# Performance work log

Measured on AMD Instinct MI355X. Metric: run time of the kernel, lower is better.

The kernel has to match this reference:

```python
import jax, jax.numpy as jnp
import numpy as np

B, L, H, E = 8, 1024, 8, 64  # self-attention: S=L, D=E
SCALE = 1.0 / np.sqrt(E).astype(np.float32)


def setup_inputs() -> dict:
    key = jax.random.key(0)
    ks = jax.random.split(key, 6)
    shp = (B, L, H, E)
    names = ["q_re", "q_im", "k_re", "k_im", "v_re", "v_im"]
    return {n: jax.random.normal(k, shp, dtype=jnp.float32) for n, k in zip(names, ks)}


def reference(q_re, q_im, k_re, k_im, v_re, v_im):
    q = jax.lax.complex(q_re, q_im)  # [B,L,H,E] complex64
    k = jax.lax.complex(k_re, k_im)  # [B,S,H,E] complex64
    # complex QK^T (no conjugate, matching torch einsum semantics)
    scores = jnp.einsum('blhe,bshe->bhls', q, k)      # [B,H,L,S] complex64
    A = jax.nn.softmax(SCALE * jnp.abs(scores), axis=-1)  # [B,H,L,S] real
    # A is promoted to complex with zero imaginary part in the original;
    # multiplying complex V by a real A is equivalent per real/imag part.
    V_re = jnp.einsum('bhls,bshd->blhd', A, v_re)     # [B,L,H,D]
    V_im = jnp.einsum('bhls,bshd->blhd', A, v_im)     # [B,L,H,D]
    return jnp.stack([V_re, V_im], axis=-1)           # [B,L,H,D,2] (re, im)
```

## Files before the change

### kernel.cpp

```cpp
#include <hip/hip_runtime.h>


#define B_ 8
#define L_ 1024
#define H_ 8
#define E_ 64
#define SB 64
#define QB 128
#define NT 16
#define IMG_BYTES 32768
#define WS_NEEDED (64ull * NT * IMG_BYTES)
#define C_EXP 0.18033688011112042f

typedef float  f32x4  __attribute__((ext_vector_type(4)));
typedef float  f32x16 __attribute__((ext_vector_type(16)));
typedef __bf16 bf16x8 __attribute__((ext_vector_type(8)));
typedef unsigned short u16x8 __attribute__((ext_vector_type(8)));
typedef unsigned short u16x4 __attribute__((ext_vector_type(4)));
typedef unsigned int   u32x4 __attribute__((ext_vector_type(4)));

static __device__ __forceinline__ unsigned short f2b(float f) {
    __bf16 h = (__bf16)f;
    return __builtin_bit_cast(unsigned short, h);
}

static __device__ __forceinline__ float fsqrt_(float x) {
    return __builtin_amdgcn_sqrtf(x);
}
static __device__ __forceinline__ float fexp2_(float x) {
    return __builtin_amdgcn_exp2f(x);
}

static __device__ __forceinline__ u16x8 pack8(float4 a, float4 b) {
    u16x8 t;
    t[0]=f2b(a.x); t[1]=f2b(a.y); t[2]=f2b(a.z); t[3]=f2b(a.w);
    t[4]=f2b(b.x); t[5]=f2b(b.y); t[6]=f2b(b.z); t[7]=f2b(b.w);
    return t;
}

static __device__ __forceinline__ f32x16 mfma32(u16x8 a, u16x8 b, f32x16 c) {
    return __builtin_amdgcn_mfma_f32_32x32x16_bf16(
        __builtin_bit_cast(bf16x8, a), __builtin_bit_cast(bf16x8, b), c, 0, 0, 0);
}

static __device__ __forceinline__ unsigned int cvtpk(float lo, float hi) {
    unsigned int r;
    asm("v_cvt_pk_bf16_f32 %0, %1, %2" : "=v"(r) : "v"(lo), "v"(hi));
    return r;
}

static __device__ __forceinline__ void plswap(unsigned int& x, unsigned int& y) {
    asm("v_permlane32_swap_b32 %0, %1" : "+v"(x), "+v"(y));
}

static __device__ __forceinline__ u16x8 negbf8(u16x8 a) {
    u32x4 u = __builtin_bit_cast(u32x4, a);
    u[0] ^= 0x80008000u; u[1] ^= 0x80008000u; u[2] ^= 0x80008000u; u[3] ^= 0x80008000u;
    return __builtin_bit_cast(u16x8, u);
}

static __device__ __forceinline__ void qk_half(
    const u16x8 K[8], const u16x8 qre[4], const u16x8 qim[4],
    f32x16& sR, f32x16& sI)
{
    const f32x16 z16 = {};
    __builtin_amdgcn_s_setprio(1);
    sR = mfma32(K[0], qre[0], z16);
    sI = mfma32(K[1], qre[0], z16);
    sR = mfma32(K[1], negbf8(qim[0]), sR);
    sI = mfma32(K[0], qim[0], sI);
    sR = mfma32(K[2], qre[1], sR);
    sI = mfma32(K[3], qre[1], sI);
    sR = mfma32(K[3], negbf8(qim[1]), sR);
    sI = mfma32(K[2], qim[1], sI);
    sR = mfma32(K[4], qre[2], sR);
    sI = mfma32(K[5], qre[2], sI);
    sR = mfma32(K[5], negbf8(qim[2]), sR);
    sI = mfma32(K[4], qim[2], sI);
    sR = mfma32(K[6], qre[3], sR);
    sI = mfma32(K[7], qre[3], sI);
    sR = mfma32(K[7], negbf8(qim[3]), sR);
    sI = mfma32(K[6], qim[3], sI);
    __builtin_amdgcn_s_setprio(0);
}

static __device__ __forceinline__ void sm_half(
    f32x16 sR, f32x16 sI, float& lsum, u16x8& pa0, u16x8& pa1)
{
    float p[16];
#pragma unroll
    for (int r = 0; r < 16; ++r) {
        float mag = fsqrt_(fmaf(sR[r], sR[r], sI[r] * sI[r]));
        p[r] = fexp2_(mag * C_EXP);
    }
    lsum += (((p[0]+p[1])+(p[2]+p[3])) + ((p[4]+p[5])+(p[6]+p[7])))
          + (((p[8]+p[9])+(p[10]+p[11])) + ((p[12]+p[13])+(p[14]+p[15])));

    unsigned int a0 = cvtpk(p[0],  p[1]),  a1 = cvtpk(p[4],  p[5]);
    unsigned int a2 = cvtpk(p[2],  p[3]),  a3 = cvtpk(p[6],  p[7]);
    unsigned int b0 = cvtpk(p[8],  p[9]),  b1 = cvtpk(p[12], p[13]);
    unsigned int b2 = cvtpk(p[10], p[11]), b3 = cvtpk(p[14], p[15]);
    plswap(a0, a1);
    plswap(a2, a3);
    plswap(b0, b1);
    plswap(b2, b3);
    u32x4 wa = {a0, a2, a1, a3};
    u32x4 wb = {b0, b2, b1, b3};
    pa0 = __builtin_bit_cast(u16x8, wa);
    pa1 = __builtin_bit_cast(u16x8, wb);
}

static __device__ __forceinline__ void pv_half(
    u16x8 pa0, u16x8 pa1, const u16x8 vf[8],
    f32x16& oR0, f32x16& oR1, f32x16& oI0, f32x16& oI1)
{
    __builtin_amdgcn_s_setprio(1);
    oR0 = mfma32(pa0, vf[0], oR0);
    oR1 = mfma32(pa0, vf[1], oR1);
    oI0 = mfma32(pa0, vf[2], oI0);
    oI1 = mfma32(pa0, vf[3], oI1);
    oR0 = mfma32(pa1, vf[4], oR0);
    oR1 = mfma32(pa1, vf[5], oR1);
    oI0 = mfma32(pa1, vf[6], oI0);
    oI1 = mfma32(pa1, vf[7], oI1);
    __builtin_amdgcn_s_setprio(0);
}

__global__ __launch_bounds__(256) void ffa_prepack(
    const float* __restrict__ k_re, const float* __restrict__ k_im,
    const float* __restrict__ v_re, const float* __restrict__ v_im,
    char* __restrict__ ws)
{
    const int tid = threadIdx.x;
    const int bh  = blockIdx.x >> 4;
    const int st  = blockIdx.x & 15;
    const int b   = bh >> 3;
    const int h   = bh & 7;
    const int s0  = st * SB;
    char* const img = ws + (size_t)blockIdx.x * IMG_BYTES;

    const int l   = tid & 63;
    const int fg  = tid >> 6;
    const int l31 = l & 31;
    const int lh  = l >> 5;

#pragma unroll
    for (int ff = 0; ff < 8; ++ff) {
        const int f = fg * 8 + ff;
        u16x8 val;
        if (f < 16) {
            const int kh = f >> 3, ks = (f >> 1) & 3, c = f & 1;
            const float* src = (c ? k_im : k_re)
                + ((size_t)((b * L_ + s0 + kh * 32 + l31) * H_ + h)) * E_ + ks * 16 + lh * 8;
            const float4* p = (const float4*)src;
            val = pack8(p[0], p[1]);
        } else {
            const int g = f - 16, ks = g >> 2, j = g & 3;
            const float* src = (j >= 2) ? v_im : v_re;
            const int d = (j & 1) * 32 + l31;
            const int sb = s0 + ks * 16 + lh * 8;
            float4 t0, t1;
            t0.x = src[((size_t)((b * L_ + sb + 0) * H_ + h)) * E_ + d];
            t0.y = src[((size_t)((b * L_ + sb + 1) * H_ + h)) * E_ + d];
            t0.z = src[((size_t)((b * L_ + sb + 2) * H_ + h)) * E_ + d];
            t0.w = src[((size_t)((b * L_ + sb + 3) * H_ + h)) * E_ + d];
            t1.x = src[((size_t)((b * L_ + sb + 4) * H_ + h)) * E_ + d];
            t1.y = src[((size_t)((b * L_ + sb + 5) * H_ + h)) * E_ + d];
            t1.z = src[((size_t)((b * L_ + sb + 6) * H_ + h)) * E_ + d];
            t1.w = src[((size_t)((b * L_ + sb + 7) * H_ + h)) * E_ + d];
            val = pack8(t0, t1);
        }
        *(u16x8*)(img + f * 1024 + l * 16) = val;
    }
}

__global__ __launch_bounds__(256, 2) void ffa_main(
    const float* __restrict__ q_re, const float* __restrict__ q_im,
    const char* __restrict__ ws, float* __restrict__ out)
{
    const int tid  = threadIdx.x;
    const int lane = tid & 63;
    const int w    = tid >> 6;
    const int l31  = lane & 31;
    const int h    = lane >> 5;

    const int work = (blockIdx.x & 7) * 64 + (blockIdx.x >> 3);
    const int bh   = work >> 3;
    const int qblk = work & 7;
    const int b    = bh >> 3;
    const int hh   = bh & 7;
    const char* const imgs = ws + (size_t)bh * (NT * IMG_BYTES) + lane * 16;

    u16x8 kc[8], kn[8], vf[8];
#pragma unroll
    for (int j = 0; j < 8; ++j)
        kc[j] = *(const u16x8*)(imgs + j * 1024);
    __builtin_amdgcn_sched_barrier(0);

    u16x8 qre[4], qim[4];
    {
        const int qrow = qblk * QB + w * 32 + l31;
        const int base = ((b * L_ + qrow) * H_ + hh) * E_;
#pragma unroll
        for (int ks = 0; ks < 4; ++ks) {
            const float4* pr = (const float4*)(q_re + base + ks * 16 + h * 8);
            const float4* pi = (const float4*)(q_im + base + ks * 16 + h * 8);
            qre[ks] = pack8(pr[0], pr[1]);
            qim[ks] = pack8(pi[0], pi[1]);
        }
    }

    f32x16 oR0 = {}, oR1 = {}, oI0 = {}, oI1 = {};
    float lsum = 0.f;

    for (int t = 0; t < NT; ++t) {
        const char* const tb0 = imgs + (size_t)t * IMG_BYTES;
        const char* const tb1 = tb0 + IMG_BYTES;

#pragma unroll
        for (int g = 0; g < 8; ++g)
            vf[g] = *(const u16x8*)(tb0 + (16 + g) * 1024);
#pragma unroll
        for (int j = 0; j < 8; ++j)
            kn[j] = *(const u16x8*)(tb0 + 8192 + j * 1024);
        __builtin_amdgcn_sched_barrier(0);
        {
            f32x16 sR, sI;
            qk_half(kc, qre, qim, sR, sI);
            u16x8 pa0, pa1;
            sm_half(sR, sI, lsum, pa0, pa1);
            pv_half(pa0, pa1, vf, oR0, oR1, oI0, oI1);
        }

#pragma unroll
        for (int g = 0; g < 8; ++g)
            vf[g] = *(const u16x8*)(tb0 + (24 + g) * 1024);
        if (t < NT - 1) {
#pragma unroll
            for (int j = 0; j < 8; ++j)
                kc[j] = *(const u16x8*)(tb1 + j * 1024);
        }
        __builtin_amdgcn_sched_barrier(0);
        {
            f32x16 sR, sI;
            qk_half(kn, qre, qim, sR, sI);
            u16x8 pa0, pa1;
            sm_half(sR, sI, lsum, pa0, pa1);
            pv_half(pa0, pa1, vf, oR0, oR1, oI0, oI1);
        }
    }

    lsum += __shfl_xor(lsum, 32);
    const float inv = 1.0f / lsum;
#pragma unroll
    for (int r = 0; r < 16; ++r) {
        const int qs = (r & 3) + 8 * (r >> 2) + 4 * h;
        const float iv = __shfl(inv, qs);
        const int lq = qblk * QB + w * 32 + qs;
        float* op = out + ((b * L_ + lq) * H_ + hh) * (E_ * 2);
        float2 v0 = make_float2(oR0[r] * iv, oI0[r] * iv);
        float2 v1 = make_float2(oR1[r] * iv, oI1[r] * iv);
        *(float2*)(op + l31 * 2)      = v0;
        *(float2*)(op + 64 + l31 * 2) = v1;
    }
}

__global__ __launch_bounds__(256) void ffa_fwd_fb(
    const float* __restrict__ q_re, const float* __restrict__ q_im,
    const float* __restrict__ k_re, const float* __restrict__ k_im,
    const float* __restrict__ v_re, const float* __restrict__ v_im,
    float* __restrict__ out)
{
    __shared__ __align__(16) unsigned short Kt[64 * 128];
    __shared__ __align__(16) unsigned short Vt[128 * 64];
    __shared__ __align__(16) unsigned short Pw[4 * 16 * 64];
    char* const kb = (char*)Kt;
    char* const vb = (char*)Vt;

    const int tid  = threadIdx.x;
    const int lane = tid & 63;
    const int w    = tid >> 6;
    const int lr   = lane & 15;
    const int lg   = lane >> 4;
    const int lg16 = lg * 16;
    const int qblk = blockIdx.x & 15;
    const int bh   = blockIdx.x >> 4;
    const int b    = bh >> 3;
    const int h    = bh & 7;

    u16x8 qre[2], qim[2], qimn[2];
    {
        const int qrow = qblk * 64 + w * 16 + lr;
        const int base = ((b * L_ + qrow) * H_ + h) * E_ + lg * 8;
#pragma unroll
        for (int ks = 0; ks < 2; ++ks) {
            const float4* pr = (const float4*)(q_re + base + ks * 32);
            const float4* pi = (const float4*)(q_im + base + ks * 32);
            qre[ks] = pack8(pr[0], pr[1]);
            qim[ks] = pack8(pi[0], pi[1]);
#pragma unroll
            for (int i = 0; i < 8; ++i)
                qimn[ks][i] = (unsigned short)(qim[ks][i] ^ 0x8000u);
        }
    }

    float lsum[4];
    f32x4 Ore[4], Oim[4];
    const f32x4 zero = {0.f, 0.f, 0.f, 0.f};
#pragma unroll
    for (int r = 0; r < 4; ++r) lsum[r] = 0.f;
#pragma unroll
    for (int dt = 0; dt < 4; ++dt) { Ore[dt] = zero; Oim[dt] = zero; }

    const int sr = tid >> 2;
    const int sc = (tid & 3) * 16;
    const int vtens = tid >> 7;
    const int vd    = ((tid >> 4) & 7) * 8;
    const int vs    = (tid & 15) * 4;
    const float* const vsrc = vtens ? v_im : v_re;

    for (int st = 0; st < L_ / SB; ++st) {
        const int s0 = st * SB;
        {
            const int kg = ((b * L_ + s0 + sr) * H_ + h) * E_ + sc;
            const float4* pr = (const float4*)(k_re + kg);
            const float4* pi = (const float4*)(k_im + kg);
            float4 r0 = pr[0], r1 = pr[1], r2 = pr[2], r3 = pr[3];
            float4 i0 = pi[0], i1 = pi[1], i2 = pi[2], i3 = pi[3];
            const int krow = sr * 256;
            const int ksw  = (sr & 7) << 4;
            *(u16x8*)(kb + ((krow + sc * 2           ) ^ ksw)) = pack8(r0, r1);
            *(u16x8*)(kb + ((krow + sc * 2 + 16      ) ^ ksw)) = pack8(r2, r3);
            *(u16x8*)(kb + ((krow + 128 + sc * 2     ) ^ ksw)) = pack8(i0, i1);
            *(u16x8*)(kb + ((krow + 128 + sc * 2 + 16) ^ ksw)) = pack8(i2, i3);
        }
        {
            float vv[4][8];
#pragma unroll
            for (int j = 0; j < 4; ++j) {
                const float4* p = (const float4*)(vsrc + ((b * L_ + s0 + vs + j) * H_ + h) * E_ + vd);
                float4 x = p[0], y = p[1];
                vv[j][0]=x.x; vv[j][1]=x.y; vv[j][2]=x.z; vv[j][3]=x.w;
                vv[j][4]=y.x; vv[j][5]=y.y; vv[j][6]=y.z; vv[j][7]=y.w;
            }
#pragma unroll
            for (int i = 0; i < 8; ++i) {
                const int row = vtens * 64 + vd + i;
                u16x4 t;
                t[0]=f2b(vv[0][i]); t[1]=f2b(vv[1][i]); t[2]=f2b(vv[2][i]); t[3]=f2b(vv[3][i]);
                *(u16x4*)(vb + ((row * 128 + vs * 2) ^ ((row & 7) << 4))) = t;
            }
        }
        __syncthreads();

        f32x4 aR[4], aI[4];
#pragma unroll
        for (int t = 0; t < 4; ++t) { aR[t] = zero; aI[t] = zero; }
#pragma unroll
        for (int t = 0; t < 4; ++t) {
            const int key = t * 16 + lr;
            const char* kr = kb + key * 256;
            const int sw = (key & 7) << 4;
            u16x8 br0 = *(const u16x8*)(kr + (( lg16      ) ^ sw));
            u16x8 br1 = *(const u16x8*)(kr + (( 64 + lg16 ) ^ sw));
            u16x8 bi0 = *(const u16x8*)(kr + ((128 + lg16 ) ^ sw));
            u16x8 bi1 = *(const u16x8*)(kr + ((192 + lg16 ) ^ sw));
            aR[t] = __builtin_amdgcn_mfma_f32_16x16x32_bf16(__builtin_bit_cast(bf16x8,qre[0]),  __builtin_bit_cast(bf16x8,br0), aR[t],0,0,0);
            aR[t] = __builtin_amdgcn_mfma_f32_16x16x32_bf16(__builtin_bit_cast(bf16x8,qre[1]),  __builtin_bit_cast(bf16x8,br1), aR[t],0,0,0);
            aR[t] = __builtin_amdgcn_mfma_f32_16x16x32_bf16(__builtin_bit_cast(bf16x8,qimn[0]), __builtin_bit_cast(bf16x8,bi0), aR[t],0,0,0);
            aR[t] = __builtin_amdgcn_mfma_f32_16x16x32_bf16(__builtin_bit_cast(bf16x8,qimn[1]), __builtin_bit_cast(bf16x8,bi1), aR[t],0,0,0);
            aI[t] = __builtin_amdgcn_mfma_f32_16x16x32_bf16(__builtin_bit_cast(bf16x8,qre[0]),  __builtin_bit_cast(bf16x8,bi0), aI[t],0,0,0);
            aI[t] = __builtin_amdgcn_mfma_f32_16x16x32_bf16(__builtin_bit_cast(bf16x8,qre[1]),  __builtin_bit_cast(bf16x8,bi1), aI[t],0,0,0);
            aI[t] = __builtin_amdgcn_mfma_f32_16x16x32_bf16(__builtin_bit_cast(bf16x8,qim[0]),  __builtin_bit_cast(bf16x8,br0), aI[t],0,0,0);
            aI[t] = __builtin_amdgcn_mfma_f32_16x16x32_bf16(__builtin_bit_cast(bf16x8,qim[1]),  __builtin_bit_cast(bf16x8,br1), aI[t],0,0,0);
        }

        float p_[4][4];
#pragma unroll
        for (int t = 0; t < 4; ++t)
#pragma unroll
            for (int r = 0; r < 4; ++r) {
                float re = aR[t][r], im = aI[t][r];
                p_[t][r] = fexp2_(fsqrt_(fmaf(re, re, im * im)) * C_EXP);
            }
#pragma unroll
        for (int r = 0; r < 4; ++r)
            lsum[r] += (p_[0][r] + p_[1][r]) + (p_[2][r] + p_[3][r]);

        char* const pb = (char*)Pw + w * 2048;
#pragma unroll
        for (int t = 0; t < 4; ++t)
#pragma unroll
            for (int r = 0; r < 4; ++r) {
                const int prow = lg * 4 + r;
                *(unsigned short*)(pb + ((prow * 128 + (t * 16 + lr) * 2) ^ ((prow & 7) << 4)))
                    = f2b(p_[t][r]);
            }
        asm volatile("s_waitcnt lgkmcnt(0)" ::: "memory");
        __builtin_amdgcn_sched_barrier(0);
        const int psw = (lr & 7) << 4;
        u16x8 pf0 = *(const u16x8*)(pb + ((lr * 128 + lg16     ) ^ psw));
        u16x8 pf1 = *(const u16x8*)(pb + ((lr * 128 + 64 + lg16) ^ psw));

#pragma unroll
        for (int dt = 0; dt < 4; ++dt) {
            const int dr = dt * 16 + lr;
            const int swr = (dr & 7) << 4;
            const char* vrre = vb + dr * 128;
            const char* vrim = vb + (64 + dr) * 128;
            u16x8 vr0 = *(const u16x8*)(vrre + (( lg16     ) ^ swr));
            u16x8 vr1 = *(const u16x8*)(vrre + (( 64 + lg16) ^ swr));
            u16x8 vi0 = *(const u16x8*)(vrim + (( lg16     ) ^ swr));
            u16x8 vi1 = *(const u16x8*)(vrim + (( 64 + lg16) ^ swr));
            Ore[dt] = __builtin_amdgcn_mfma_f32_16x16x32_bf16(__builtin_bit_cast(bf16x8,pf0), __builtin_bit_cast(bf16x8,vr0), Ore[dt],0,0,0);
            Ore[dt] = __builtin_amdgcn_mfma_f32_16x16x32_bf16(__builtin_bit_cast(bf16x8,pf1), __builtin_bit_cast(bf16x8,vr1), Ore[dt],0,0,0);
            Oim[dt] = __builtin_amdgcn_mfma_f32_16x16x32_bf16(__builtin_bit_cast(bf16x8,pf0), __builtin_bit_cast(bf16x8,vi0), Oim[dt],0,0,0);
            Oim[dt] = __builtin_amdgcn_mfma_f32_16x16x32_bf16(__builtin_bit_cast(bf16x8,pf1), __builtin_bit_cast(bf16x8,vi1), Oim[dt],0,0,0);
        }
        __syncthreads();
    }

#pragma unroll
    for (int r = 0; r < 4; ++r) {
        float s = lsum[r];
        s += __shfl_xor(s, 1);
        s += __shfl_xor(s, 2);
        s += __shfl_xor(s, 4);
        s += __shfl_xor(s, 8);
        const float inv = 1.0f / s;
        const int lq = qblk * 64 + w * 16 + lg * 4 + r;
        const int obase = (((b * L_ + lq) * H_ + h) * E_) * 2;
#pragma unroll
        for (int dt = 0; dt < 4; ++dt) {
            const int d = dt * 16 + lr;
            float2 val = make_float2(Ore[dt][r] * inv, Oim[dt][r] * inv);
            *(float2*)(out + obase + d * 2) = val;
        }
    }
}

extern "C" void kernel_launch(void* const* d_in, const int* in_sizes, int n_in,
                              void* d_out, int out_size, void* d_ws, size_t ws_size,
                              hipStream_t stream) {
    const float* q_re = (const float*)d_in[0];
    const float* q_im = (const float*)d_in[1];
    const float* k_re = (const float*)d_in[2];
    const float* k_im = (const float*)d_in[3];
    const float* v_re = (const float*)d_in[4];
    const float* v_im = (const float*)d_in[5];
    float* out = (float*)d_out;

    if (ws_size >= WS_NEEDED) {
        char* ws = (char*)d_ws;
        hipLaunchKernelGGL(ffa_prepack, dim3(B_ * H_ * NT), dim3(256), 0, stream,
                           k_re, k_im, v_re, v_im, ws);
        hipLaunchKernelGGL(ffa_main, dim3(B_ * H_ * (L_ / QB)), dim3(256), 0, stream,
                           q_re, q_im, (const char*)ws, out);
    } else {
        hipLaunchKernelGGL(ffa_fwd_fb, dim3(B_ * H_ * (L_ / 64)), dim3(256), 0, stream,
                           q_re, q_im, k_re, k_im, v_re, v_im, out);
    }
}
```

Before: 87.40 us.

## Stage K/V tile images through double-buffered LDS via direct global-to-LDS loads

Each 32KB K/V tile image is now staged into a double-buffered shared-memory array using global_load_lds, so the block fetches it from global memory once. The four waves then read their K and V fragments from LDS, replacing the per-wave global loads that fetched the same tile four times. The next tile is prefetched while the current one is computed, with a vmcnt wait and a block barrier at the end of each iteration. The cost is 64KB of LDS per block, which may limit the two-blocks-per-CU occupancy target, plus a full block barrier on every tile.

```diff
diff --git a/kernel.cpp b/kernel.cpp
--- a/kernel.cpp
+++ b/kernel.cpp
@@ -57,6 +57,13 @@
     u32x4 u = __builtin_bit_cast(u32x4, a);
     u[0] ^= 0x80008000u; u[1] ^= 0x80008000u; u[2] ^= 0x80008000u; u[3] ^= 0x80008000u;
     return __builtin_bit_cast(u16x8, u);
+}
+
+static __device__ __forceinline__ void gload16(const void* g, void* l) {
+    __builtin_amdgcn_global_load_lds(
+        (const __attribute__((address_space(1))) void*)g,
+        (__attribute__((address_space(3))) void*)l,
+        16, 0, 0);
 }
 
 static __device__ __forceinline__ void qk_half(
@@ -178,6 +185,8 @@
     const float* __restrict__ q_re, const float* __restrict__ q_im,
     const char* __restrict__ ws, float* __restrict__ out)
 {
+    __shared__ __align__(16) char Buf[2][IMG_BYTES];
+
     const int tid  = threadIdx.x;
     const int lane = tid & 63;
     const int w    = tid >> 6;
@@ -189,13 +198,11 @@
     const int qblk = work & 7;
     const int b    = bh >> 3;
     const int hh   = bh & 7;
-    const char* const imgs = ws + (size_t)bh * (NT * IMG_BYTES) + lane * 16;
-
-    u16x8 kc[8], kn[8], vf[8];
+    const char* const imgt = ws + (size_t)bh * (NT * IMG_BYTES);
+
 #pragma unroll
     for (int j = 0; j < 8; ++j)
-        kc[j] = *(const u16x8*)(imgs + j * 1024);
-    __builtin_amdgcn_sched_barrier(0);
+        gload16(imgt + j * 4096 + tid * 16, Buf[0] + j * 4096 + tid * 16);
 
     u16x8 qre[4], qim[4];
     {
@@ -213,41 +220,52 @@
     f32x16 oR0 = {}, oR1 = {}, oI0 = {}, oI1 = {};
     float lsum = 0.f;
 
+    asm volatile("s_waitcnt vmcnt(0)" ::: "memory");
+    __syncthreads();
+
     for (int t = 0; t < NT; ++t) {
-        const char* const tb0 = imgs + (size_t)t * IMG_BYTES;
-        const char* const tb1 = tb0 + IMG_BYTES;
-
-#pragma unroll
-        for (int g = 0; g < 8; ++g)
-            vf[g] = *(const u16x8*)(tb0 + (16 + g) * 1024);
+        const int cur = t & 1;
+        if (t + 1 < NT) {
+            const char* src = imgt + (size_t)(t + 1) * IMG_BYTES;
+            char* dst = Buf[cur ^ 1];
+#pragma unroll
+            for (int j = 0; j < 8; ++j)
+                gload16(src + j * 4096 + tid * 16, dst + j * 4096 + tid * 16);
+        }
+        const char* const kb = Buf[cur] + lane * 16;
+
+        u16x8 kf[8], vf[8];
+
 #pragma unroll
         for (int j = 0; j < 8; ++j)
-            kn[j] = *(const u16x8*)(tb0 + 8192 + j * 1024);
-        __builtin_amdgcn_sched_barrier(0);
+            kf[j] = *(const u16x8*)(kb + j * 1024);
         {
             f32x16 sR, sI;
-            qk_half(kc, qre, qim, sR, sI);
+            qk_half(kf, qre, qim, sR, sI);
+#pragma unroll
+            for (int g = 0; g < 8; ++g)
+                vf[g] = *(const u16x8*)(kb + (16 + g) * 1024);
             u16x8 pa0, pa1;
             sm_half(sR, sI, lsum, pa0, pa1);
             pv_half(pa0, pa1, vf, oR0, oR1, oI0, oI1);
         }
 
 #pragma unroll
-        for (int g = 0; g < 8; ++g)
-            vf[g] = *(const u16x8*)(tb0 + (24 + g) * 1024);
-        if (t < NT - 1) {
-#pragma unroll
-            for (int j = 0; j < 8; ++j)
-                kc[j] = *(const u16x8*)(tb1 + j * 1024);
-        }
-        __builtin_amdgcn_sched_barrier(0);
+        for (int j = 0; j < 8; ++j)
+            kf[j] = *(const u16x8*)(kb + 8192 + j * 1024);
         {
             f32x16 sR, sI;
-            qk_half(kn, qre, qim, sR, sI);
+            qk_half(kf, qre, qim, sR, sI);
+#pragma unroll
+            for (int g = 0; g < 8; ++g)
+                vf[g] = *(const u16x8*)(kb + (24 + g) * 1024);
             u16x8 pa0, pa1;
             sm_half(sR, sI, lsum, pa0, pa1);
             pv_half(pa0, pa1, vf, oR0, oR1, oI0, oI1);
         }
+
+        asm volatile("s_waitcnt vmcnt(0)" ::: "memory");
+        __syncthreads();
     }
 
     lsum += __shfl_xor(lsum, 32);
```

After: 83.23 us. 1.05x faster.
